# Performance work log

Measured on AMD Instinct MI355X. Metric: run time of the kernel, lower is better.

## Reference

```python
import jax, jax.numpy as jnp
import numpy as np

B = 4096      # number of queries
N = 65536     # number of reference points

def setup_inputs() -> dict:
    key = jax.random.key(0)
    k1, k2, k3 = jax.random.split(key, 3)
    x = jax.random.normal(k1, (B,), dtype=jnp.float32)
    input_tensor = jax.random.normal(k2, (N,), dtype=jnp.float32)
    accuracy_tensor = jax.random.uniform(k3, (N,), dtype=jnp.float32)
    return {"x": x, "input_tensor": input_tensor, "accuracy_tensor": accuracy_tensor}

def reference(x, input_tensor, accuracy_tensor):
    # (B, N) broadcast abs-difference distance matrix
    distances = jnp.abs(input_tensor[None, :] - x[:, None])
    # nearest reference point per query
    min_idx = jnp.argmin(distances, axis=1)          # (B,)
    return accuracy_tensor[min_idx]                  # (B,)
```

## Files before the change

### kernel.cpp

```cpp
#include <hip/hip_runtime.h>

#define CHUNK 512
#define GRP   32
#define QB    4

__global__ __launch_bounds__(256, 8)
void nn_init_kernel(unsigned long long* __restrict__ best, int B) {
    int i = blockIdx.x * 256 + threadIdx.x;
    if (i < B) best[i] = ~0ULL;
}

__global__ __launch_bounds__(256, 8)
void nn_main_kernel(const float* __restrict__ x,
                    const float* __restrict__ pts,
                    unsigned long long* __restrict__ best,
                    int qg_shift)
{
    __shared__ float lds[CHUNK];
    const int tid = threadIdx.x;
    const int nqg_mask = (1 << qg_shift) - 1;
    const int qg = blockIdx.x & nqg_mask;
    const int ck = blockIdx.x >> qg_shift;

    reinterpret_cast<float2*>(lds)[tid] =
        reinterpret_cast<const float2*>(pts)[ck * (CHUNK / 2) + tid];
    __syncthreads();

    const int lane = tid & 63;
    const int wv   = tid >> 6;
    const int q    = (qg << 8) + (wv << 6) + lane;
    const float xq = x[q];

    const float inf = __builtin_inff();
    float bdA = inf, bdB = inf, prev = inf;
    int grp = 0;

    const float4* __restrict__ l4 = reinterpret_cast<const float4*>(lds);

    #pragma unroll 2
    for (int g = 0; g < CHUNK / GRP; ++g) {
        #pragma unroll
        for (int t = 0; t < GRP / 4; ++t) {
            float4 v = l4[g * (GRP / 4) + t];
            float d0 = v.x - xq;
            float d1 = v.y - xq;
            float d2 = v.z - xq;
            float d3 = v.w - xq;
            bdA = fminf(fminf(fabsf(d0), fabsf(d1)), bdA);
            bdB = fminf(fminf(fabsf(d2), fabsf(d3)), bdB);
        }
        float cur = fminf(bdA, bdB);
        grp  = (cur < prev) ? g : grp;
        prev = cur;
    }

    const float bd = prev;

    int bi = 0;
    #pragma unroll
    for (int t = GRP / 4 - 1; t >= 0; --t) {
        float4 v = l4[grp * (GRP / 4) + t];
        bi = (fabsf(v.w - xq) == bd) ? 4 * t + 3 : bi;
        bi = (fabsf(v.z - xq) == bd) ? 4 * t + 2 : bi;
        bi = (fabsf(v.y - xq) == bd) ? 4 * t + 1 : bi;
        bi = (fabsf(v.x - xq) == bd) ? 4 * t + 0 : bi;
    }

    const unsigned gidx = (unsigned)(ck * CHUNK + grp * GRP + bi);
    const unsigned long long key =
        ((unsigned long long)__float_as_uint(bd) << 32) | gidx;
    atomicMin(&best[q], key);
}

__global__ __launch_bounds__(256, 8)
void nn_gather_kernel(const unsigned long long* __restrict__ best,
                      const float* __restrict__ acc,
                      float* __restrict__ out, int B) {
    int i = blockIdx.x * 256 + threadIdx.x;
    if (i < B) out[i] = acc[(unsigned)(best[i] & 0xffffffffULL)];
}

__global__ __launch_bounds__(256, 4)
void nn_kernel(const float* __restrict__ x,
               const float* __restrict__ pts,
               const float* __restrict__ acc,
               float* __restrict__ out,
               int B, int N) {
    const int lane = threadIdx.x & 63;
    const int wave = threadIdx.x >> 6;
    const int q    = blockIdx.x * QB + wave;
    if (q >= B) return;

    const float xq = x[q];
    const int G = N >> 2;
    const int J = G >> 6;

    float bd0 = __builtin_inff(), bd1 = __builtin_inff(),
          bd2 = __builtin_inff(), bd3 = __builtin_inff();
    int   bj0 = 0, bj1 = 0, bj2 = 0, bj3 = 0;

    const float4* __restrict__ p4 = reinterpret_cast<const float4*>(pts);

    #pragma unroll 4
    for (int j = 0; j < J; ++j) {
        float4 v = p4[lane + 64 * j];
        float d0 = fabsf(v.x - xq);
        float d1 = fabsf(v.y - xq);
        float d2 = fabsf(v.z - xq);
        float d3 = fabsf(v.w - xq);
        if (d0 < bd0) { bd0 = d0; bj0 = j; }
        if (d1 < bd1) { bd1 = d1; bj1 = j; }
        if (d2 < bd2) { bd2 = d2; bj2 = j; }
        if (d3 < bd3) { bd3 = d3; bj3 = j; }
    }

    unsigned long long key;
    {
        unsigned i0 = (unsigned)(4 * (lane + 64 * bj0) + 0);
        unsigned i1 = (unsigned)(4 * (lane + 64 * bj1) + 1);
        unsigned i2 = (unsigned)(4 * (lane + 64 * bj2) + 2);
        unsigned i3 = (unsigned)(4 * (lane + 64 * bj3) + 3);
        unsigned long long k0 = ((unsigned long long)__float_as_uint(bd0) << 32) | i0;
        unsigned long long k1 = ((unsigned long long)__float_as_uint(bd1) << 32) | i1;
        unsigned long long k2 = ((unsigned long long)__float_as_uint(bd2) << 32) | i2;
        unsigned long long k3 = ((unsigned long long)__float_as_uint(bd3) << 32) | i3;
        key = k0 < k1 ? k0 : k1;
        unsigned long long k23 = k2 < k3 ? k2 : k3;
        key = key < k23 ? key : k23;
    }

    for (int i = J * 256 + lane; i < N; i += 64) {
        float d = fabsf(pts[i] - xq);
        unsigned long long k = ((unsigned long long)__float_as_uint(d) << 32) | (unsigned)i;
        key = key < k ? key : k;
    }

    #pragma unroll
    for (int off = 1; off < 64; off <<= 1) {
        unsigned long long o = __shfl_xor(key, off, 64);
        key = key < o ? key : o;
    }

    if (lane == 0) {
        out[q] = acc[(unsigned)(key & 0xffffffffULL)];
    }
}

extern "C" void kernel_launch(void* const* d_in, const int* in_sizes, int n_in,
                              void* d_out, int out_size, void* d_ws, size_t ws_size,
                              hipStream_t stream) {
    const float* x   = (const float*)d_in[0];
    const float* pts = (const float*)d_in[1];
    const float* acc = (const float*)d_in[2];
    float* out = (float*)d_out;
    const int B = in_sizes[0];
    const int N = in_sizes[1];

    const int nqg = B >> 8;
    const bool pow2 = (nqg > 0) && ((nqg & (nqg - 1)) == 0);
    const bool fast = pow2 && (B % 256 == 0) && (N % CHUNK == 0) &&
                      d_ws != nullptr && ws_size >= (size_t)B * 8;

    if (fast) {
        int qg_shift = 0;
        while ((1 << qg_shift) < nqg) ++qg_shift;
        const int nchunk = N / CHUNK;
        unsigned long long* best = (unsigned long long*)d_ws;

        hipLaunchKernelGGL(nn_init_kernel, dim3(nqg), dim3(256), 0, stream,
                           best, B);
        hipLaunchKernelGGL(nn_main_kernel, dim3(nchunk * nqg), dim3(256), 0,
                           stream, x, pts, best, qg_shift);
        hipLaunchKernelGGL(nn_gather_kernel, dim3(nqg), dim3(256), 0, stream,
                           best, acc, out, B);
    } else {
        const int blocks = (B + QB - 1) / QB;
        hipLaunchKernelGGL(nn_kernel, dim3(blocks), dim3(256), 0, stream,
                           x, pts, acc, out, B, N);
    }
}
```

Baseline: 71.78 us.

## Read reference chunk via wave-uniform scalar loads instead of LDS staging

Drops the shared-memory staging and __syncthreads in the main kernel. Each wave now independently handles one 64-query group against one chunk, with the chunk index made wave-uniform through readfirstlane, so point loads can become scalar (SMEM) loads broadcast to all lanes. The grid is remapped from block-per-(query-group, chunk) to wave-per-(query-wave, chunk). This removes LDS traffic and block barriers, but relies on the compiler emitting scalar loads and on the scalar cache keeping the chunk resident.

```diff
diff --git a/kernel.cpp b/kernel.cpp
--- a/kernel.cpp
+++ b/kernel.cpp
@@ -14,40 +14,33 @@
 void nn_main_kernel(const float* __restrict__ x,
                     const float* __restrict__ pts,
                     unsigned long long* __restrict__ best,
-                    int qg_shift)
+                    int qw_shift)
 {
-    __shared__ float lds[CHUNK];
-    const int tid = threadIdx.x;
-    const int nqg_mask = (1 << qg_shift) - 1;
-    const int qg = blockIdx.x & nqg_mask;
-    const int ck = blockIdx.x >> qg_shift;
+    const int lane = threadIdx.x & 63;
+    const int wv = __builtin_amdgcn_readfirstlane((int)(threadIdx.x >> 6));
+    const int w  = blockIdx.x * 4 + wv;
+    const int qw = w & ((1 << qw_shift) - 1);
+    const int ck = w >> qw_shift;
 
-    reinterpret_cast<float2*>(lds)[tid] =
-        reinterpret_cast<const float2*>(pts)[ck * (CHUNK / 2) + tid];
-    __syncthreads();
+    const int q = (qw << 6) + lane;
+    const float xq = x[q];
 
-    const int lane = tid & 63;
-    const int wv   = tid >> 6;
-    const int q    = (qg << 8) + (wv << 6) + lane;
-    const float xq = x[q];
+    const float* __restrict__ pc = pts + (size_t)(unsigned)ck * CHUNK;
 
     const float inf = __builtin_inff();
     float bdA = inf, bdB = inf, prev = inf;
     int grp = 0;
 
-    const float4* __restrict__ l4 = reinterpret_cast<const float4*>(lds);
-
     #pragma unroll 2
     for (int g = 0; g < CHUNK / GRP; ++g) {
         #pragma unroll
         for (int t = 0; t < GRP / 4; ++t) {
-            float4 v = l4[g * (GRP / 4) + t];
-            float d0 = v.x - xq;
-            float d1 = v.y - xq;
-            float d2 = v.z - xq;
-            float d3 = v.w - xq;
-            bdA = fminf(fminf(fabsf(d0), fabsf(d1)), bdA);
-            bdB = fminf(fminf(fabsf(d2), fabsf(d3)), bdB);
+            float p0 = pc[g * GRP + 4 * t + 0];
+            float p1 = pc[g * GRP + 4 * t + 1];
+            float p2 = pc[g * GRP + 4 * t + 2];
+            float p3 = pc[g * GRP + 4 * t + 3];
+            bdA = fminf(fminf(fabsf(p0 - xq), fabsf(p1 - xq)), bdA);
+            bdB = fminf(fminf(fabsf(p2 - xq), fabsf(p3 - xq)), bdB);
         }
         float cur = fminf(bdA, bdB);
         grp  = (cur < prev) ? g : grp;
@@ -56,10 +49,12 @@
 
     const float bd = prev;
 
+    const float4* __restrict__ pg =
+        reinterpret_cast<const float4*>(pc + grp * GRP);
     int bi = 0;
     #pragma unroll
     for (int t = GRP / 4 - 1; t >= 0; --t) {
-        float4 v = l4[grp * (GRP / 4) + t];
+        float4 v = pg[t];
         bi = (fabsf(v.w - xq) == bd) ? 4 * t + 3 : bi;
         bi = (fabsf(v.z - xq) == bd) ? 4 * t + 2 : bi;
         bi = (fabsf(v.y - xq) == bd) ? 4 * t + 1 : bi;
@@ -156,23 +151,23 @@
     const int B = in_sizes[0];
     const int N = in_sizes[1];
 
-    const int nqg = B >> 8;
-    const bool pow2 = (nqg > 0) && ((nqg & (nqg - 1)) == 0);
-    const bool fast = pow2 && (B % 256 == 0) && (N % CHUNK == 0) &&
+    const int nqw = B >> 6;
+    const int nchunk = N / CHUNK;
+    const bool pow2 = (nqw > 0) && ((nqw & (nqw - 1)) == 0);
+    const bool fast = pow2 && (B % 64 == 0) && (N % CHUNK == 0) &&
                       d_ws != nullptr && ws_size >= (size_t)B * 8;
 
     if (fast) {
-        int qg_shift = 0;
-        while ((1 << qg_shift) < nqg) ++qg_shift;
-        const int nchunk = N / CHUNK;
+        int qw_shift = 0;
+        while ((1 << qw_shift) < nqw) ++qw_shift;
         unsigned long long* best = (unsigned long long*)d_ws;
 
-        hipLaunchKernelGGL(nn_init_kernel, dim3(nqg), dim3(256), 0, stream,
-                           best, B);
-        hipLaunchKernelGGL(nn_main_kernel, dim3(nchunk * nqg), dim3(256), 0,
-                           stream, x, pts, best, qg_shift);
-        hipLaunchKernelGGL(nn_gather_kernel, dim3(nqg), dim3(256), 0, stream,
-                           best, acc, out, B);
+        hipLaunchKernelGGL(nn_init_kernel, dim3((B + 255) / 256), dim3(256), 0,
+                           stream, best, B);
+        hipLaunchKernelGGL(nn_main_kernel, dim3((nchunk * nqw) / 4), dim3(256),
+                           0, stream, x, pts, best, qw_shift);
+        hipLaunchKernelGGL(nn_gather_kernel, dim3((B + 255) / 256), dim3(256),
+                           0, stream, best, acc, out, B);
     } else {
         const int blocks = (B + QB - 1) / QB;
         hipLaunchKernelGGL(nn_kernel, dim3(blocks), dim3(256), 0, stream,
```

Result: slower. 73.45 us (+2.3%).
